# Performance work log

Hardware: AMD Instinct MI355X
Metric: run time of the kernel (lower is better)

The kernel has to match this reference:

```python
import jax, jax.numpy as jnp
import numpy as np

B, S, D, H = 2, 2048, 1024, 16
HEAD_DIM = D // H  # 64


def setup_inputs() -> dict:
    key = jax.random.key(0)
    ks = jax.random.split(key, 7)
    x = jax.random.normal(ks[0], (B, S, D), dtype=jnp.float32)
    W_q = jax.random.normal(ks[1], (D, D), dtype=jnp.float32) * 0.02
    W_k = jax.random.normal(ks[2], (D, D), dtype=jnp.float32) * 0.02
    W_v = jax.random.normal(ks[3], (D, D), dtype=jnp.float32) * 0.02
    W_o = jax.random.normal(ks[4], (D, D), dtype=jnp.float32) * 0.02 / np.sqrt(2 * 12)
    b_o = jnp.zeros((D,), dtype=jnp.float32)
    # Ragged prefix attention_mask: per-row valid lengths in [S/2, S];
    # row 0 forced to full length so max_valid_len == S statically (jit-safe).
    lengths = jax.random.randint(ks[5], (B,), S // 2, S + 1)
    lengths = lengths.at[0].set(S)
    attention_mask = (jnp.arange(S)[None, :] < lengths[:, None]).astype(jnp.float32)
    return {"x": x, "attention_mask": attention_mask, "W_q": W_q, "W_k": W_k,
            "W_v": W_v, "W_o": W_o, "b_o": b_o}


def reference(x, attention_mask, W_q, W_k, W_v, W_o, b_o):
    b, s, d = x.shape
    h, hd = H, HEAD_DIM
    # QKV projections (no bias, qkv_bias=False)
    q = (x @ W_q.T).reshape(b, s, h, hd).transpose(0, 2, 1, 3)  # [b,h,s,hd]
    # Masking keys/values at invalid (padded) positions; for prefix masks this
    # is exactly the module's per-batch packing loop (max_valid_len == s).
    m = attention_mask[:, None, :, None]  # [b,1,s,1]
    k = ((x @ W_k.T).reshape(b, s, h, hd).transpose(0, 2, 1, 3)) * m
    v = ((x @ W_v.T).reshape(b, s, h, hd).transpose(0, 2, 1, 3)) * m
    # Naive causal attention, same op order as the torch module:
    # mask with -inf first, then scale by 1/sqrt(head_dim), then softmax.
    causal = jnp.triu(jnp.ones((s, s), dtype=bool), 1)  # True above diagonal
    scores = jnp.einsum('bhqd,bhkd->bhqk', q, k)
    scores = jnp.where(causal[None, None], -jnp.inf, scores)
    att = jax.nn.softmax(scores / jnp.sqrt(jnp.float32(hd)), axis=-1)
    ctx = jnp.einsum('bhqk,bhkd->bhqd', att, v)  # [b,h,s,hd]
    ctx = ctx.transpose(0, 2, 1, 3).reshape(b, s, d)
    # Output projection (dropout is inference no-op)
    return ctx @ W_o.T + b_o
```

## Files before the change

kernel.cpp:

```cpp
#include <hip/hip_runtime.h>

#define B_  2
#define S_  2048
#define D_  1024
#define H_  16
#define HD_ 64
#define N3_ 3072
#define M_  4096

typedef _Float16 f16;
typedef _Float16 f16x2 __attribute__((ext_vector_type(2)));
typedef _Float16 f16x4 __attribute__((ext_vector_type(4)));
typedef _Float16 f16x8 __attribute__((ext_vector_type(8)));
typedef float    f32x4 __attribute__((ext_vector_type(4)));

__device__ __forceinline__ void async16(const f16* g, f16* l) {
  __builtin_amdgcn_global_load_lds(
      (const __attribute__((address_space(1))) unsigned int*)g,
      (__attribute__((address_space(3))) unsigned int*)l, 16, 0, 0);
}

__device__ __forceinline__ f16x2 pkrtz(float a, float b) {
  return __builtin_bit_cast(f16x2, __builtin_amdgcn_cvt_pkrtz(a, b));
}

__device__ __forceinline__ float vexp2(float x) {
  float r; asm("v_exp_f32 %0, %1" : "=v"(r) : "v"(x)); return r;
}

__global__ __launch_bounds__(256)
void cvt_all(const float* __restrict__ x,
             const float* __restrict__ Wq, const float* __restrict__ Wk,
             const float* __restrict__ Wv, const float* __restrict__ Wo,
             f16* __restrict__ xb, f16* __restrict__ wdst, float qscale) {
  const int i = blockIdx.x * 256 + threadIdx.x;
  const int XN4 = M_ * D_ / 4;
  const int WN4 = D_ * D_ / 4;
  const float* src;
  f16* dst;
  float scale = 1.0f;
  int j;
  if (i < XN4) {
    src = x; dst = xb; j = i;
  } else {
    int k = i - XN4;
    int m = k >> 18;
    j = k & (WN4 - 1);
    src = (m == 0) ? Wq : (m == 1) ? Wk : (m == 2) ? Wv : Wo;
    if (m == 0) scale = qscale;
    dst = wdst + (size_t)m * D_ * D_;
  }
  float4 v = ((const float4*)src)[j];
  f16x4 o = { (f16)(v.x * scale), (f16)(v.y * scale),
              (f16)(v.z * scale), (f16)(v.w * scale) };
  ((f16x4*)dst)[j] = o;
}

__global__ __launch_bounds__(256)
void gemm_qkv(const f16* __restrict__ A, const f16* __restrict__ Bw,
              f16* __restrict__ Cq, f16* __restrict__ vtout,
              const float* __restrict__ mask) {
  __shared__ f16 As[128 * 64];
  __shared__ f16 Bs[128 * 64];

  const int tid  = threadIdx.x;
  const int lane = tid & 63;
  const int w    = tid >> 6;
  const int lcol = lane & 15;
  const int quad = lane >> 4;
  const int lx   = lcol & 7;
  const int wave_m = w >> 1, wave_n = w & 1;

  const int m0 = blockIdx.y * 128;
  const int n0 = blockIdx.x * 128;

  const int rr  = lane >> 3;
  const int gch = (lane & 7) ^ rr;

  const f16* gA[4];
  const f16* gB[4];
  f16* lA[4];
  f16* lB[4];
#pragma unroll
  for (int i = 0; i < 4; i++) {
    int seg = i * 4 + w;
    int row = seg * 8 + rr;
    gA[i] = A  + (size_t)(m0 + row) * D_ + gch * 8;
    gB[i] = Bw + (size_t)(n0 + row) * D_ + gch * 8;
    lA[i] = As + seg * 512;
    lB[i] = Bs + seg * 512;
  }

  int offA[4], offB[4];
#pragma unroll
  for (int i = 0; i < 4; i++) {
    offA[i] = (wave_m * 64 + i * 16 + lcol) * 64;
    offB[i] = (wave_n * 64 + i * 16 + lcol) * 64;
  }

  const f32x4 zero = {0.f, 0.f, 0.f, 0.f};
  f32x4 acc[4][4];
#pragma unroll
  for (int i = 0; i < 4; i++)
#pragma unroll
    for (int j = 0; j < 4; j++) acc[i][j] = zero;

  for (int k0 = 0; k0 < D_; k0 += 64) {
    __syncthreads();
#pragma unroll
    for (int i = 0; i < 4; i++) async16(gA[i] + k0, lA[i]);
#pragma unroll
    for (int i = 0; i < 4; i++) async16(gB[i] + k0, lB[i]);
    __syncthreads();

#pragma unroll
    for (int ks = 0; ks < 2; ks++) {
      const int co = ((quad + 4 * ks) ^ lx) * 8;
      f16x8 af[4], bf[4];
#pragma unroll
      for (int i = 0; i < 4; i++) af[i] = *(const f16x8*)(As + offA[i] + co);
#pragma unroll
      for (int i = 0; i < 4; i++) bf[i] = *(const f16x8*)(Bs + offB[i] + co);
#pragma unroll
      for (int mi = 0; mi < 4; mi++)
#pragma unroll
        for (int ni = 0; ni < 4; ni++)
          acc[mi][ni] = __builtin_amdgcn_mfma_f32_16x16x32_f16(
              af[mi], bf[ni], acc[mi][ni], 0, 0, 0);
    }
  }

  if (n0 >= 2 * D_) {
#pragma unroll
    for (int mi = 0; mi < 4; mi++) {
      const int mgb = m0 + wave_m * 64 + mi * 16 + quad * 4;
      const int b = mgb >> 11, s = mgb & (S_ - 1);
      const float mk0 = mask[mgb], mk1 = mask[mgb + 1];
      const float mk2 = mask[mgb + 2], mk3 = mask[mgb + 3];
#pragma unroll
      for (int ni = 0; ni < 4; ni++) {
        const int vcol = n0 - 2 * D_ + wave_n * 64 + ni * 16 + lcol;
        f16x4 v = { (f16)(acc[mi][ni][0] * mk0), (f16)(acc[mi][ni][1] * mk1),
                    (f16)(acc[mi][ni][2] * mk2), (f16)(acc[mi][ni][3] * mk3) };
        *(f16x4*)(vtout +
                  ((size_t)(b * 16 + (vcol >> 6)) * 64 + (vcol & 63)) * S_ + s) = v;
      }
    }
  } else {
    const bool kmask = (n0 >= D_);
#pragma unroll
    for (int mi = 0; mi < 4; mi++) {
#pragma unroll
      for (int r = 0; r < 4; r++) {
        int mg = m0 + wave_m * 64 + mi * 16 + quad * 4 + r;
        float mk = kmask ? mask[mg] : 1.0f;
#pragma unroll
        for (int ni = 0; ni < 4; ni++) {
          int ng = n0 + wave_n * 64 + ni * 16 + lcol;
          Cq[(size_t)mg * N3_ + ng] = (f16)(acc[mi][ni][r] * mk);
        }
      }
    }
  }
}

__global__ __launch_bounds__(256)
void gemm_proj(const f16* __restrict__ A, const f16* __restrict__ Bw,
               float* __restrict__ Cf, const float* __restrict__ bias) {
  __shared__ f16 As[64 * 64];
  __shared__ f16 Bs[128 * 64];

  const int tid  = threadIdx.x;
  const int lane = tid & 63;
  const int w    = tid >> 6;
  const int lcol = lane & 15;
  const int quad = lane >> 4;
  const int lx   = lcol & 7;
  const int wave_m = w >> 1, wave_n = w & 1;

  const int m0 = blockIdx.y * 64;
  const int n0 = blockIdx.x * 128;

  const int rr  = lane >> 3;
  const int gch = (lane & 7) ^ rr;

  const f16* gA[2];
  const f16* gB[4];
  f16* lA[2];
  f16* lB[4];
#pragma unroll
  for (int i = 0; i < 2; i++) {
    int seg = 2 * w + i;
    gA[i] = A + (size_t)(m0 + seg * 8 + rr) * D_ + gch * 8;
    lA[i] = As + seg * 512;
  }
#pragma unroll
  for (int i = 0; i < 4; i++) {
    int seg = i * 4 + w;
    gB[i] = Bw + (size_t)(n0 + seg * 8 + rr) * D_ + gch * 8;
    lB[i] = Bs + seg * 512;
  }

  int offA[2], offB[4];
#pragma unroll
  for (int i = 0; i < 2; i++) offA[i] = (wave_m * 32 + i * 16 + lcol) * 64;
#pragma unroll
  for (int i = 0; i < 4; i++) offB[i] = (wave_n * 64 + i * 16 + lcol) * 64;

  const f32x4 zero = {0.f, 0.f, 0.f, 0.f};
  f32x4 acc[2][4];
#pragma unroll
  for (int i = 0; i < 2; i++)
#pragma unroll
    for (int j = 0; j < 4; j++) acc[i][j] = zero;

  for (int k0 = 0; k0 < D_; k0 += 64) {
    __syncthreads();
#pragma unroll
    for (int i = 0; i < 2; i++) async16(gA[i] + k0, lA[i]);
#pragma unroll
    for (int i = 0; i < 4; i++) async16(gB[i] + k0, lB[i]);
    __syncthreads();

#pragma unroll
    for (int ks = 0; ks < 2; ks++) {
      const int co = ((quad + 4 * ks) ^ lx) * 8;
      f16x8 af[2], bf[4];
#pragma unroll
      for (int i = 0; i < 2; i++) af[i] = *(const f16x8*)(As + offA[i] + co);
#pragma unroll
      for (int i = 0; i < 4; i++) bf[i] = *(const f16x8*)(Bs + offB[i] + co);
#pragma unroll
      for (int mi = 0; mi < 2; mi++)
#pragma unroll
        for (int ni = 0; ni < 4; ni++)
          acc[mi][ni] = __builtin_amdgcn_mfma_f32_16x16x32_f16(
              af[mi], bf[ni], acc[mi][ni], 0, 0, 0);
    }
  }

#pragma unroll
  for (int mi = 0; mi < 2; mi++) {
#pragma unroll
    for (int r = 0; r < 4; r++) {
      int mg = m0 + wave_m * 32 + mi * 16 + quad * 4 + r;
#pragma unroll
      for (int ni = 0; ni < 4; ni++) {
        int ng = n0 + wave_n * 64 + ni * 16 + lcol;
        Cf[(size_t)mg * D_ + ng] = acc[mi][ni][r] + bias[ng];
      }
    }
  }
}

__global__ __launch_bounds__(128)
void flash_attn8(const f16* __restrict__ qkv, const f16* __restrict__ vt,
                 f16* __restrict__ ctx, float* __restrict__ part) {
  __shared__ f16 Ks[64 * 64];
  __shared__ f16 Vs[64 * 64];

  const int tid  = threadIdx.x;
  const int lane = tid & 63;
  const int w    = tid >> 6;
  const int lcol = lane & 15;
  const int quad = lane >> 4;
  const int lx   = lcol & 7;

  const int id   = blockIdx.x;
  const int bh   = (id & 7) + 8 * ((id >> 3) & 3);
  const int u    = id >> 5;
  const int p    = u & 15;
  const int role = u >> 4;
  const int g    = 31 - p;
  const int b    = bh >> 4, h = bh & 15;

  const int rsub = lane >> 3;
  const int gch  = (lane & 7) ^ rsub;
  const f16* Kg = qkv + (size_t)b * S_ * N3_ + D_ + h * HD_;
  const f16* Vg = vt + (size_t)bh * HD_ * S_;

  int srow[4];
  f16 *ldsK[4], *ldsV[4];
#pragma unroll
  for (int i = 0; i < 4; i++) {
    const int r0 = w * 32 + i * 8;
    srow[i] = r0 + rsub;
    ldsK[i] = Ks + r0 * 64;
    ldsV[i] = Vs + r0 * 64;
  }

  const f32x4 zero = {0.f, 0.f, 0.f, 0.f};
  f32x4 o0[4], o1[4];
  float lp0, lp1;

  auto run = [&](int qt, int ktb, int kte) {
    const int qrow0 = qt * 64 + w * 32 + lcol;
    const int qrow1 = qrow0 + 16;
    const f16* Qp0 = qkv + (size_t)(b * S_ + qrow0) * N3_ + h * HD_;
    const f16* Qp1 = qkv + (size_t)(b * S_ + qrow1) * N3_ + h * HD_;
    const f16x8 qa0 = *(const f16x8*)(Qp0 + quad * 8);
    const f16x8 qa1 = *(const f16x8*)(Qp0 + 32 + quad * 8);
    const f16x8 qb0 = *(const f16x8*)(Qp1 + quad * 8);
    const f16x8 qb1 = *(const f16x8*)(Qp1 + 32 + quad * 8);
#pragma unroll
    for (int i = 0; i < 4; i++) { o0[i] = zero; o1[i] = zero; }
    lp0 = 0.f; lp1 = 0.f;

    for (int kt = ktb; kt < kte; kt++) {
      const int kbase = kt * 64;
      __syncthreads();
#pragma unroll
      for (int i = 0; i < 4; i++)
        async16(Kg + (size_t)(kbase + srow[i]) * N3_ + gch * 8, ldsK[i]);
#pragma unroll
      for (int i = 0; i < 4; i++)
        async16(Vg + (size_t)srow[i] * S_ + kbase + gch * 8, ldsV[i]);
      __syncthreads();

      f32x4 sc0[4], sc1[4];
#pragma unroll
      for (int ct = 0; ct < 4; ct++) {
        const f16* kr = Ks + (ct * 16 + lcol) * 64;
        f16x8 kf0 = *(const f16x8*)(kr + ((quad    ) ^ lx) * 8);
        f16x8 kf1 = *(const f16x8*)(kr + ((quad + 4) ^ lx) * 8);
        f32x4 z0 = zero;
        z0 = __builtin_amdgcn_mfma_f32_16x16x32_f16(kf0, qa0, z0, 0, 0, 0);
        z0 = __builtin_amdgcn_mfma_f32_16x16x32_f16(kf1, qa1, z0, 0, 0, 0);
        sc0[ct] = z0;
        f32x4 z1 = zero;
        z1 = __builtin_amdgcn_mfma_f32_16x16x32_f16(kf0, qb0, z1, 0, 0, 0);
        z1 = __builtin_amdgcn_mfma_f32_16x16x32_f16(kf1, qb1, z1, 0, 0, 0);
        sc1[ct] = z1;
      }

      if (kt == qt) {
        const int qoff0 = w * 32 + lcol;
        const int qoff1 = qoff0 + 16;
#pragma unroll
        for (int ct = 0; ct < 4; ct++) {
          const int koff = ct * 16 + quad * 4;
#pragma unroll
          for (int r = 0; r < 4; r++) {
            if (koff + r > qoff0) sc0[ct][r] = -1e30f;
            if (koff + r > qoff1) sc1[ct][r] = -1e30f;
          }
        }
      }

      f16x4 pf0[4], pf1[4];
#pragma unroll
      for (int ct = 0; ct < 4; ct++) {
        float a0 = vexp2(sc0[ct][0]), a1 = vexp2(sc0[ct][1]);
        float a2 = vexp2(sc0[ct][2]), a3 = vexp2(sc0[ct][3]);
        lp0 += (a0 + a1) + (a2 + a3);
        f16x2 alo = pkrtz(a0, a1);
        f16x2 ahi = pkrtz(a2, a3);
        f16x4 pa = { alo[0], alo[1], ahi[0], ahi[1] };
        pf0[ct] = pa;
        float b0 = vexp2(sc1[ct][0]), b1 = vexp2(sc1[ct][1]);
        float b2 = vexp2(sc1[ct][2]), b3 = vexp2(sc1[ct][3]);
        lp1 += (b0 + b1) + (b2 + b3);
        f16x2 blo = pkrtz(b0, b1);
        f16x2 bhi = pkrtz(b2, b3);
        f16x4 pb = { blo[0], blo[1], bhi[0], bhi[1] };
        pf1[ct] = pb;
      }

#pragma unroll
      for (int ht = 0; ht < 4; ht++) {
        const f16* vr = Vs + (ht * 16 + lcol) * 64 + (quad & 1) * 4;
#pragma unroll
        for (int ct = 0; ct < 4; ct++) {
          f16x4 vf = *(const f16x4*)(vr + (((2 * ct + (quad >> 1)) ^ lx) * 8));
          o0[ht] = __builtin_amdgcn_mfma_f32_16x16x16f16(vf, pf0[ct], o0[ht], 0, 0, 0);
          o1[ht] = __builtin_amdgcn_mfma_f32_16x16x16f16(vf, pf1[ct], o1[ht], 0, 0, 0);
        }
      }
    }
    lp0 += __shfl_xor(lp0, 16);
    lp0 += __shfl_xor(lp0, 32);
    lp1 += __shfl_xor(lp1, 16);
    lp1 += __shfl_xor(lp1, 32);
  };

  const int row0 = w * 32 + lcol;
  const int row1 = row0 + 16;

  if (role == 0) {
    run(g, 0, 16);
    float* slot = part + ((size_t)(bh * 16 + p) * 2 + 0) * 4160;
#pragma unroll
    for (int ht = 0; ht < 4; ht++) {
      *(f32x4*)(slot + row0 * 64 + ht * 16 + quad * 4) = o0[ht];
      *(f32x4*)(slot + row1 * 64 + ht * 16 + quad * 4) = o1[ht];
    }
    if (quad == 0) {
      slot[4096 + row0] = lp0;
      slot[4096 + row1] = lp1;
    }
  } else {
    run(g, 16, g + 1);
    float* slot = part + ((size_t)(bh * 16 + p) * 2 + 1) * 4160;
#pragma unroll
    for (int ht = 0; ht < 4; ht++) {
      *(f32x4*)(slot + row0 * 64 + ht * 16 + quad * 4) = o0[ht];
      *(f32x4*)(slot + row1 * 64 + ht * 16 + quad * 4) = o1[ht];
    }
    if (quad == 0) {
      slot[4096 + row0] = lp0;
      slot[4096 + row1] = lp1;
    }

    run(p, 0, p + 1);
    const float inv0 = 1.f / lp0;
    const float inv1 = 1.f / lp1;
    f16* cp0 = ctx + (size_t)(b * S_ + p * 64 + row0) * D_ + h * HD_ + quad * 4;
    f16* cp1 = ctx + (size_t)(b * S_ + p * 64 + row1) * D_ + h * HD_ + quad * 4;
#pragma unroll
    for (int ht = 0; ht < 4; ht++) {
      f16x4 ov0 = { (f16)(o0[ht][0] * inv0), (f16)(o0[ht][1] * inv0),
                    (f16)(o0[ht][2] * inv0), (f16)(o0[ht][3] * inv0) };
      *(f16x4*)(cp0 + ht * 16) = ov0;
      f16x4 ov1 = { (f16)(o1[ht][0] * inv1), (f16)(o1[ht][1] * inv1),
                    (f16)(o1[ht][2] * inv1), (f16)(o1[ht][3] * inv1) };
      *(f16x4*)(cp1 + ht * 16) = ov1;
    }
  }
}

__global__ __launch_bounds__(256)
void attn_combine(const float* __restrict__ part, f16* __restrict__ ctx) {
  const int sid = blockIdx.x;
  const int bh  = sid >> 4, p = sid & 15;
  const int g   = 31 - p;
  const int b   = bh >> 4, h = bh & 15;
  const int t   = threadIdx.x;
  const int row = t >> 2;
  const int c0  = (t & 3) * 16;

  const float* sA = part + ((size_t)sid * 2 + 0) * 4160;
  const float* sB = part + ((size_t)sid * 2 + 1) * 4160;
  const float inv = 1.f / (sA[4096 + row] + sB[4096 + row]);
  const int qrow = g * 64 + row;
  f16* cp = ctx + (size_t)(b * S_ + qrow) * D_ + h * HD_ + c0;
#pragma unroll
  for (int j0 = 0; j0 < 16; j0 += 4) {
    f32x4 a  = *(const f32x4*)(sA + row * 64 + c0 + j0);
    f32x4 bb = *(const f32x4*)(sB + row * 64 + c0 + j0);
    f16x4 ov = { (f16)((a[0] + bb[0]) * inv), (f16)((a[1] + bb[1]) * inv),
                 (f16)((a[2] + bb[2]) * inv), (f16)((a[3] + bb[3]) * inv) };
    *(f16x4*)(cp + j0) = ov;
  }
}

extern "C" void kernel_launch(void* const* d_in, const int* in_sizes, int n_in,
                              void* d_out, int out_size, void* d_ws, size_t ws_size,
                              hipStream_t stream) {
  (void)in_sizes; (void)n_in; (void)out_size; (void)ws_size;
  const float* x  = (const float*)d_in[0];
  const float* am = (const float*)d_in[1];
  const float* Wq = (const float*)d_in[2];
  const float* Wk = (const float*)d_in[3];
  const float* Wv = (const float*)d_in[4];
  const float* Wo = (const float*)d_in[5];
  const float* bo = (const float*)d_in[6];
  float* out = (float*)d_out;

  f16* ws   = (f16*)d_ws;
  f16* wqkv = ws;
  f16* wo16 = wqkv + (size_t)3 * D_ * D_;
  f16* xb   = wo16 + (size_t)D_ * D_;
  f16* qkvb = xb + (size_t)M_ * D_;
  f16* vtb  = qkvb + (size_t)M_ * N3_;
  f16* ctxb = vtb + (size_t)M_ * D_;
  float* part = (float*)(ctxb + (size_t)M_ * D_);

  const float qscale = 0.125f * 1.4426950408889634f;

  cvt_all<<<dim3((M_ * D_ + 4 * D_ * D_) / 1024), 256, 0, stream>>>(
      x, Wq, Wk, Wv, Wo, xb, wqkv, qscale);

  gemm_qkv<<<dim3(N3_ / 128, M_ / 128), 256, 0, stream>>>(
      xb, wqkv, qkvb, vtb, am);
  flash_attn8<<<dim3(1024), 128, 0, stream>>>(qkvb, vtb, ctxb, part);
  attn_combine<<<dim3(512), 256, 0, stream>>>(part, ctxb);
  gemm_proj<<<dim3(D_ / 128, M_ / 64), 256, 0, stream>>>(
      ctxb, wo16, out, bo);
}
```

Measured before the change: 180.8 us.

## Double-buffer QKV GEMM LDS loads and remap blocks for XCD-local L2 reuse

```diff
diff --git a/kernel.cpp b/kernel.cpp
--- a/kernel.cpp
+++ b/kernel.cpp
@@ -60,8 +60,10 @@
 void gemm_qkv(const f16* __restrict__ A, const f16* __restrict__ Bw,
               f16* __restrict__ Cq, f16* __restrict__ vtout,
               const float* __restrict__ mask) {
-  __shared__ f16 As[128 * 64];
-  __shared__ f16 Bs[128 * 64];
+  __shared__ f16 As0[128 * 64];
+  __shared__ f16 Bs0[128 * 64];
+  __shared__ f16 As1[128 * 64];
+  __shared__ f16 Bs1[128 * 64];
 
   const int tid  = threadIdx.x;
   const int lane = tid & 63;
@@ -71,24 +73,24 @@
   const int lx   = lcol & 7;
   const int wave_m = w >> 1, wave_n = w & 1;
 
-  const int m0 = blockIdx.y * 128;
-  const int n0 = blockIdx.x * 128;
+  const int lin   = blockIdx.x;
+  const int xcd   = lin & 7;
+  const int chunk = lin >> 3;
+  const int mIdx  = chunk / 12;
+  const int nIdx  = chunk - mIdx * 12;
+  const int m0 = ((xcd >> 1) * 8 + mIdx) * 128;
+  const int n0 = ((xcd & 1) * 12 + nIdx) * 128;
 
   const int rr  = lane >> 3;
   const int gch = (lane & 7) ^ rr;
 
   const f16* gA[4];
   const f16* gB[4];
-  f16* lA[4];
-  f16* lB[4];
 #pragma unroll
   for (int i = 0; i < 4; i++) {
-    int seg = i * 4 + w;
-    int row = seg * 8 + rr;
+    int row = (i * 4 + w) * 8 + rr;
     gA[i] = A  + (size_t)(m0 + row) * D_ + gch * 8;
     gB[i] = Bw + (size_t)(n0 + row) * D_ + gch * 8;
-    lA[i] = As + seg * 512;
-    lB[i] = Bs + seg * 512;
   }
 
   int offA[4], offB[4];
@@ -105,22 +107,22 @@
 #pragma unroll
     for (int j = 0; j < 4; j++) acc[i][j] = zero;
 
-  for (int k0 = 0; k0 < D_; k0 += 64) {
-    __syncthreads();
-#pragma unroll
-    for (int i = 0; i < 4; i++) async16(gA[i] + k0, lA[i]);
-#pragma unroll
-    for (int i = 0; i < 4; i++) async16(gB[i] + k0, lB[i]);
-    __syncthreads();
-
+  auto stage = [&](int k0, f16* sA, f16* sB) {
+#pragma unroll
+    for (int i = 0; i < 4; i++) {
+      async16(gA[i] + k0, sA + (i * 4 + w) * 512);
+      async16(gB[i] + k0, sB + (i * 4 + w) * 512);
+    }
+  };
+  auto compute = [&](const f16* sA, const f16* sB) {
 #pragma unroll
     for (int ks = 0; ks < 2; ks++) {
       const int co = ((quad + 4 * ks) ^ lx) * 8;
       f16x8 af[4], bf[4];
 #pragma unroll
-      for (int i = 0; i < 4; i++) af[i] = *(const f16x8*)(As + offA[i] + co);
-#pragma unroll
-      for (int i = 0; i < 4; i++) bf[i] = *(const f16x8*)(Bs + offB[i] + co);
+      for (int i = 0; i < 4; i++) af[i] = *(const f16x8*)(sA + offA[i] + co);
+#pragma unroll
+      for (int i = 0; i < 4; i++) bf[i] = *(const f16x8*)(sB + offB[i] + co);
 #pragma unroll
       for (int mi = 0; mi < 4; mi++)
 #pragma unroll
@@ -128,7 +130,24 @@
           acc[mi][ni] = __builtin_amdgcn_mfma_f32_16x16x32_f16(
               af[mi], bf[ni], acc[mi][ni], 0, 0, 0);
     }
-  }
+  };
+
+  stage(0, As0, Bs0);
+  for (int it = 0; it < 14; it += 2) {
+    stage((it + 1) * 64, As1, Bs1);
+    asm volatile("s_waitcnt vmcnt(8)\ns_barrier" ::: "memory");
+    compute(As0, Bs0);
+    asm volatile("s_barrier" ::: "memory");
+    stage((it + 2) * 64, As0, Bs0);
+    asm volatile("s_waitcnt vmcnt(8)\ns_barrier" ::: "memory");
+    compute(As1, Bs1);
+    asm volatile("s_barrier" ::: "memory");
+  }
+  stage(15 * 64, As1, Bs1);
+  asm volatile("s_waitcnt vmcnt(8)\ns_barrier" ::: "memory");
+  compute(As0, Bs0);
+  asm volatile("s_waitcnt vmcnt(0)\ns_barrier" ::: "memory");
+  compute(As1, Bs1);
 
   if (n0 >= 2 * D_) {
 #pragma unroll
@@ -480,7 +499,7 @@
   cvt_all<<<dim3((M_ * D_ + 4 * D_ * D_) / 1024), 256, 0, stream>>>(
       x, Wq, Wk, Wv, Wo, xb, wqkv, qscale);
 
-  gemm_qkv<<<dim3(N3_ / 128, M_ / 128), 256, 0, stream>>>(
+  gemm_qkv<<<dim3(768), 256, 0, stream>>>(
       xb, wqkv, qkvb, vtb, am);
   flash_attn8<<<dim3(1024), 128, 0, stream>>>(qkvb, vtb, ctxb, part);
   attn_combine<<<dim3(512), 256, 0, stream>>>(part, ctxb);
```

Measured after the change: 178.8 us. No clear change (-1.1%).
